# Kernel tuning notes

Hardware: AMD Instinct MI355X
Metric: run time of the kernel (lower is better)

## Reference

```python
import jax, jax.numpy as jnp
import numpy as np

EPS_OT = 0.1        # args.model.ot_reg
N_ITERS = 5         # args.model.ot_transport
COS_EPS = 1e-8      # torch F.cosine_similarity eps
L2_EPS = 1e-12      # torch F.normalize eps
LN_EPS = 1e-5       # nn.LayerNorm default eps
IN_DIM, HID = 768, 256


def setup_inputs() -> dict:
    key = jax.random.key(0)
    ks = jax.random.split(key, 8)
    Ba, Bb, Sa, Sb = 48, 48, 96, 96
    s_in = 1.0 / np.sqrt(IN_DIM)
    return {
        "batch_a": jax.random.normal(ks[0], (Ba, Sa, IN_DIM), jnp.float32),
        "batch_b": jax.random.normal(ks[1], (Bb, Sb, IN_DIM), jnp.float32),
        "Wq": jax.random.normal(ks[2], (IN_DIM, HID), jnp.float32) * s_in,
        "bq": jnp.zeros((HID,), jnp.float32),
        "Wk": jax.random.normal(ks[3], (IN_DIM, HID), jnp.float32) * s_in,
        "bk": jnp.zeros((HID,), jnp.float32),
        "Wv": jax.random.normal(ks[4], (IN_DIM, HID), jnp.float32) * s_in,
        "bv": jnp.zeros((HID,), jnp.float32),
        "ln_g": jnp.ones((HID,), jnp.float32),
        "ln_b": jnp.zeros((HID,), jnp.float32),
    }


def _layernorm(x, g, b):
    mu = jnp.mean(x, axis=-1, keepdims=True)
    var = jnp.var(x, axis=-1, keepdims=True)
    return (x - mu) * jax.lax.rsqrt(var + LN_EPS) * g + b


def _sinkhorn(C):
    # multiplicative Sinkhorn on kernel exp(C/eps); row/col renormalization
    T = jnp.exp(C / EPS_OT)  # [Ba,Bb,Sa,Sb]
    def body(_, T):
        T = T / jnp.sum(T, axis=-1, keepdims=True)
        T = T / jnp.sum(T, axis=-2, keepdims=True)
        return T
    return jax.lax.fori_loop(0, N_ITERS, body, T)


def reference(batch_a, batch_b, Wq, bq, Wk, bk, Wv, bv, ln_g, ln_b):
    q = batch_a @ Wq + bq          # [Ba,Sa,H]
    k = batch_b @ Wk + bk          # [Bb,Sb,H]
    v = batch_b @ Wv + bv          # [Bb,Sb,H]

    # cosine similarity across batches: [Ba,Bb,Sa,Sb]
    qn = q / jnp.maximum(jnp.linalg.norm(q, axis=-1, keepdims=True), COS_EPS)
    kn = k / jnp.maximum(jnp.linalg.norm(k, axis=-1, keepdims=True), COS_EPS)
    C = jnp.einsum('aid,bjd->abij', qn, kn)

    T = jax.lax.stop_gradient(_sinkhorn(C))  # C.detach() in source
    # F.normalize(dim=-1): L2 over last dim
    T = T / jnp.maximum(jnp.linalg.norm(T, axis=-1, keepdims=True), L2_EPS)
    # dropout p=0.0 -> identity (eval)

    attended = jnp.einsum('abij,bjd->abid', T, v) + q[:, None]  # [Ba,Bb,Sa,H]
    return _layernorm(attended, ln_g, ln_b)
```

## Files before the change

kernel.cpp:

```cpp
#include <hip/hip_runtime.h>
#include <hip/hip_bf16.h>

typedef __attribute__((ext_vector_type(4))) float f32x4;
typedef __attribute__((ext_vector_type(2))) float f32x2;
typedef __attribute__((ext_vector_type(8))) short bf16x8;
typedef __attribute__((ext_vector_type(4))) short s16x4;

#define BA 48
#define BB 48
#define SS 96
#define DIN 768
#define HH 256

static __device__ __forceinline__ short f2bf(float f) {
    __hip_bfloat16 h = __float2bfloat16(f);
    return *reinterpret_cast<short*>(&h);
}

static __device__ __forceinline__ f32x4 mfma16(bf16x8 a, bf16x8 b, f32x4 c) {
    return __builtin_amdgcn_mfma_f32_16x16x32_bf16(a, b, c, 0, 0, 0);
}

__global__ __launch_bounds__(256) void wt_kernel(
    const float* __restrict__ Wq, const float* __restrict__ Wk,
    const float* __restrict__ Wv, short* __restrict__ wt) {
    __shared__ float tile[64][65];
    int k0 = blockIdx.x * 64, n0 = blockIdx.y * 64, mat = blockIdx.z;
    const float* W = (mat == 0) ? Wq : (mat == 1) ? Wk : Wv;
    int t = threadIdx.x;
#pragma unroll
    for (int j = 0; j < 16; ++j) {
        int kk = j * 4 + (t >> 6);
        int nn = t & 63;
        tile[kk][nn] = W[(size_t)(k0 + kk) * HH + n0 + nn];
    }
    __syncthreads();
#pragma unroll
    for (int j = 0; j < 4; ++j) {
        int nn = j * 16 + (t >> 4);
        int kk = (t & 15) * 4;
        s16x4 pk;
#pragma unroll
        for (int i = 0; i < 4; ++i) pk[i] = f2bf(tile[kk + i][nn]);
        *reinterpret_cast<s16x4*>(&wt[(size_t)(mat * HH + n0 + nn) * DIN + k0 + kk]) = pk;
    }
}

__global__ __launch_bounds__(384) void qkv_kernel(
    const float* __restrict__ Xa, const float* __restrict__ Xb,
    const float* __restrict__ bq, const float* __restrict__ bk, const float* __restrict__ bv,
    const short* __restrict__ wt,
    float* __restrict__ q_ws, float* __restrict__ k_ws, short* __restrict__ vt_ws) {
    __shared__ short vtile[64][104];

    int bb = blockIdx.x;
    int mat = blockIdx.y;
    int c0 = blockIdx.z * 64;
    int tid = threadIdx.x;
    int wave = tid >> 6, lane = tid & 63;
    int c = lane & 15, g = lane >> 4;

    const float* X = ((mat == 0) ? Xa : Xb) + bb * SS * DIN;
    const short* Wt = wt + mat * HH * DIN;
    const float* bias = (mat == 0) ? bq : (mat == 1) ? bk : bv;

    const f32x4 z4 = {0.f, 0.f, 0.f, 0.f};
    f32x4 acc[4];
#pragma unroll
    for (int n = 0; n < 4; ++n) acc[n] = z4;

    const float* ap = X + (16 * wave + c) * DIN + g * 8;
    const short* bp = Wt + (c0 + c) * DIN + g * 8;
    for (int kk = 0; kk < DIN; kk += 32) {
        f32x4 a0 = *reinterpret_cast<const f32x4*>(ap + kk);
        f32x4 a1 = *reinterpret_cast<const f32x4*>(ap + kk + 4);
        bf16x8 af;
        af[0] = f2bf(a0[0]); af[1] = f2bf(a0[1]); af[2] = f2bf(a0[2]); af[3] = f2bf(a0[3]);
        af[4] = f2bf(a1[0]); af[5] = f2bf(a1[1]); af[6] = f2bf(a1[2]); af[7] = f2bf(a1[3]);
#pragma unroll
        for (int n = 0; n < 4; ++n) {
            bf16x8 bf = *reinterpret_cast<const bf16x8*>(bp + n * 16 * DIN + kk);
            acc[n] = mfma16(af, bf, acc[n]);
        }
    }
#pragma unroll
    for (int n = 0; n < 4; ++n) {
        float bv_ = bias[c0 + n * 16 + c];
#pragma unroll
        for (int r = 0; r < 4; ++r) acc[n][r] += bv_;
    }

    if (mat < 2) {
        float* dst = (mat == 0) ? q_ws : k_ws;
#pragma unroll
        for (int n = 0; n < 4; ++n)
#pragma unroll
            for (int r = 0; r < 4; ++r)
                dst[(bb * SS + 16 * wave + 4 * g + r) * HH + c0 + n * 16 + c] = acc[n][r];
    } else {
#pragma unroll
        for (int n = 0; n < 4; ++n)
#pragma unroll
            for (int r = 0; r < 4; ++r)
                vtile[n * 16 + c][16 * wave + 4 * g + r] = f2bf(acc[n][r]);
        __syncthreads();
#pragma unroll
        for (int t2 = 0; t2 < 2; ++t2) {
            int t = tid + t2 * 384;
            int d = t / 12, ch = t % 12;
            bf16x8 pk = *reinterpret_cast<const bf16x8*>(&vtile[d][ch * 8]);
            *reinterpret_cast<bf16x8*>(vt_ws + ((size_t)(bb * HH) + c0 + d) * SS + ch * 8) = pk;
        }
    }
}

__global__ __launch_bounds__(256) void norm_kernel(
    const float* __restrict__ q_ws, const float* __restrict__ k_ws,
    short* __restrict__ qn_ws, short* __restrict__ kn_ws) {
    int row = blockIdx.x * 4 + (threadIdx.x >> 6);
    int lane = threadIdx.x & 63;
    int isq = (row < 4608);
    const float* src = isq ? q_ws : k_ws;
    short* dst = isq ? qn_ws : kn_ws;
    int r = isq ? row : row - 4608;

    f32x4 v = *reinterpret_cast<const f32x4*>(src + (size_t)r * HH + lane * 4);
    float s = v[0] * v[0] + v[1] * v[1] + v[2] * v[2] + v[3] * v[3];
#pragma unroll
    for (int m = 1; m < 64; m <<= 1) s += __shfl_xor(s, m);
    float inv = 1.0f / fmaxf(sqrtf(s), 1e-8f);
    s16x4 o;
#pragma unroll
    for (int j = 0; j < 4; ++j) o[j] = f2bf(v[j] * inv);
    *reinterpret_cast<s16x4*>(dst + (size_t)r * HH + lane * 4) = o;
}

__global__ __launch_bounds__(256, 2) void sink_kernel(
    const short* __restrict__ qn_ws, const short* __restrict__ kn_ws,
    short* __restrict__ t_ws, int a_off) {
    int wave = threadIdx.x >> 6, lane = threadIdx.x & 63;
    int c = lane & 15, g = lane >> 4;
    int b = blockIdx.x * 4 + wave;
    int al = blockIdx.y;
    int a = al + a_off;

    const short* qbase = qn_ws + (size_t)(a * SS) * HH + c * HH + g * 8;
    const short* kbase = kn_ws + (size_t)(b * SS) * HH + c * HH + g * 8;

    const f32x4 z4 = {0.f, 0.f, 0.f, 0.f};
    f32x4 K[6][6];
#pragma unroll
    for (int ti = 0; ti < 6; ++ti)
#pragma unroll
        for (int tj = 0; tj < 6; ++tj) K[ti][tj] = z4;

#pragma unroll
    for (int kk = 0; kk < 8; ++kk) {
        bf16x8 qf[6];
#pragma unroll
        for (int ti = 0; ti < 6; ++ti)
            qf[ti] = *reinterpret_cast<const bf16x8*>(qbase + ti * 16 * HH + kk * 32);
#pragma unroll
        for (int tj = 0; tj < 6; ++tj) {
            bf16x8 kf = *reinterpret_cast<const bf16x8*>(kbase + tj * 16 * HH + kk * 32);
#pragma unroll
            for (int ti = 0; ti < 6; ++ti)
                K[ti][tj] = mfma16(kf, qf[ti], K[ti][tj]);
        }
    }

#pragma unroll
    for (int ti = 0; ti < 6; ++ti)
#pragma unroll
        for (int tj = 0; tj < 6; ++tj)
#pragma unroll
            for (int r = 0; r < 4; ++r)
                K[ti][tj][r] = exp2f(K[ti][tj][r] * 14.4269504088896341f);

#pragma unroll 1
    for (int it = 0; it < 5; ++it) {
#pragma unroll
        for (int ti = 0; ti < 6; ++ti) {
            float rs = 0.f;
#pragma unroll
            for (int tj = 0; tj < 6; ++tj)
                rs += K[ti][tj][0] + K[ti][tj][1] + K[ti][tj][2] + K[ti][tj][3];
            rs += __shfl_xor(rs, 16);
            rs += __shfl_xor(rs, 32);
            float rinv = 1.0f / rs;
#pragma unroll
            for (int tj = 0; tj < 6; ++tj)
#pragma unroll
                for (int r = 0; r < 4; ++r) K[ti][tj][r] *= rinv;
        }
        f32x4 cs[6];
#pragma unroll
        for (int tj = 0; tj < 6; ++tj) {
            cs[tj] = K[0][tj];
#pragma unroll
            for (int ti = 1; ti < 6; ++ti)
#pragma unroll
                for (int r = 0; r < 4; ++r) cs[tj][r] += K[ti][tj][r];
        }
#pragma unroll
        for (int m = 1; m < 16; m <<= 1)
#pragma unroll
            for (int tj = 0; tj < 6; ++tj)
#pragma unroll
                for (int r = 0; r < 4; ++r) cs[tj][r] += __shfl_xor(cs[tj][r], m);
#pragma unroll
        for (int tj = 0; tj < 6; ++tj) {
#pragma unroll
            for (int r = 0; r < 4; ++r) cs[tj][r] = 1.0f / cs[tj][r];
#pragma unroll
            for (int ti = 0; ti < 6; ++ti)
#pragma unroll
                for (int r = 0; r < 4; ++r) K[ti][tj][r] *= cs[tj][r];
        }
    }

    short* tp = t_ws + (size_t)(al * BB + b) * SS * SS;
#pragma unroll
    for (int ti = 0; ti < 6; ++ti) {
        float ss = 0.f;
#pragma unroll
        for (int tj = 0; tj < 6; ++tj)
#pragma unroll
            for (int r = 0; r < 4; ++r) ss += K[ti][tj][r] * K[ti][tj][r];
        ss += __shfl_xor(ss, 16);
        ss += __shfl_xor(ss, 32);
        float linv = 1.0f / fmaxf(sqrtf(ss), 1e-12f);
#pragma unroll
        for (int tj = 0; tj < 6; ++tj) {
            s16x4 pk;
#pragma unroll
            for (int r = 0; r < 4; ++r) pk[r] = f2bf(K[ti][tj][r] * linv);
            *reinterpret_cast<s16x4*>(tp + (16 * ti + c) * SS + 16 * tj + 4 * g) = pk;
        }
    }
}

__global__ __launch_bounds__(768, 6) void pv_kernel(
    const short* __restrict__ t_ws, const short* __restrict__ vt_ws,
    const float* __restrict__ q_ws,
    const float* __restrict__ ln_g, const float* __restrict__ ln_b,
    float* __restrict__ out, int a_off) {
    __shared__ float stats[2][2][SS];
    __shared__ float etile[12][4][136];

    int b = blockIdx.x, al = blockIdx.y;
    int a = al + a_off;
    int tid = threadIdx.x;
    int wave = tid >> 6, lane = tid & 63;
    int rt = wave % 6, h = wave / 6;
    int c = lane & 15, g = lane >> 4;

    const f32x4 z4 = {0.f, 0.f, 0.f, 0.f};
    f32x4 acc[8];
#pragma unroll
    for (int n = 0; n < 8; ++n) acc[n] = z4;

    const short* tp = t_ws + ((size_t)(al * BB + b)) * SS * SS + (16 * rt + c) * SS + g * 8;
    const short* vp = vt_ws + ((size_t)(b * HH) + 128 * h + c) * SS + g * 8;
#pragma unroll
    for (int ks = 0; ks < 3; ++ks) {
        bf16x8 af = *reinterpret_cast<const bf16x8*>(tp + ks * 32);
#pragma unroll
        for (int n = 0; n < 8; ++n) {
            bf16x8 bf = *reinterpret_cast<const bf16x8*>(vp + n * 16 * SS + ks * 32);
            acc[n] = mfma16(af, bf, acc[n]);
        }
    }

    const float* qa = q_ws + (size_t)a * SS * HH + 128 * h;
    int r0 = 16 * rt + 4 * g;
    float s1[4] = {0.f, 0.f, 0.f, 0.f};
    float s2[4] = {0.f, 0.f, 0.f, 0.f};
#pragma unroll
    for (int n = 0; n < 8; ++n)
#pragma unroll
        for (int r = 0; r < 4; ++r) {
            float x = acc[n][r] + qa[(r0 + r) * HH + n * 16 + c];
            acc[n][r] = x;
            s1[r] += x;
            s2[r] += x * x;
        }
#pragma unroll
    for (int m = 1; m < 16; m <<= 1)
#pragma unroll
        for (int r = 0; r < 4; ++r) {
            s1[r] += __shfl_xor(s1[r], m);
            s2[r] += __shfl_xor(s2[r], m);
        }
    if (c == 0) {
#pragma unroll
        for (int r = 0; r < 4; ++r) {
            stats[h][0][r0 + r] = s1[r];
            stats[h][1][r0 + r] = s2[r];
        }
    }
    __syncthreads();
    float mean[4], inv[4];
#pragma unroll
    for (int r = 0; r < 4; ++r) {
        float t1 = stats[0][0][r0 + r] + stats[1][0][r0 + r];
        float t2 = stats[0][1][r0 + r] + stats[1][1][r0 + r];
        mean[r] = t1 * (1.0f / 256.0f);
        float var = t2 * (1.0f / 256.0f) - mean[r] * mean[r];
        inv[r] = rsqrtf(var + 1e-5f);
    }

    f32x2 g2 = *reinterpret_cast<const f32x2*>(ln_g + 128 * h + 2 * lane);
    f32x2 b2 = *reinterpret_cast<const f32x2*>(ln_b + 128 * h + 2 * lane);
    float* ob = out + ((size_t)(a * BB + b)) * SS * HH + 128 * h;
#pragma unroll
    for (int r = 0; r < 4; ++r) {
#pragma unroll
        for (int n = 0; n < 8; ++n)
            etile[wave][g][n * 16 + c] = (acc[n][r] - mean[r]) * inv[r];
#pragma unroll
        for (int t = 0; t < 4; ++t) {
            f32x2 x2 = *reinterpret_cast<const f32x2*>(&etile[wave][t][2 * lane]);
            *reinterpret_cast<f32x2*>(ob + (size_t)(16 * rt + 4 * t + r) * HH + 2 * lane) =
                x2 * g2 + b2;
        }
    }
}

extern "C" void kernel_launch(void* const* d_in, const int* in_sizes, int n_in,
                              void* d_out, int out_size, void* d_ws, size_t ws_size,
                              hipStream_t stream) {
    const float* Xa = (const float*)d_in[0];
    const float* Xb = (const float*)d_in[1];
    const float* Wq = (const float*)d_in[2];
    const float* bq = (const float*)d_in[3];
    const float* Wk = (const float*)d_in[4];
    const float* bk = (const float*)d_in[5];
    const float* Wv = (const float*)d_in[6];
    const float* bv = (const float*)d_in[7];
    const float* ln_g = (const float*)d_in[8];
    const float* ln_b = (const float*)d_in[9];
    float* out = (float*)d_out;

    char* ws = (char*)d_ws;
    short* wt    = (short*)(ws);
    float* q_ws  = (float*)(ws + 1179648);
    float* k_ws  = (float*)(ws + 5898240);
    short* qn_ws = (short*)(ws + 10616832);
    short* kn_ws = (short*)(ws + 12976128);
    short* vt_ws = (short*)(ws + 15335424);

    const size_t t_full = (size_t)BA * BB * SS * SS * 2;
    size_t t_off = 17694720;
    size_t avail = (ws_size > t_off) ? ws_size - t_off : 0;
    int nch;
    if (avail >= t_full) nch = 1;
    else if (avail >= t_full / 2) nch = 2;
    else if (avail >= t_full / 4) nch = 4;
    else if (avail >= t_full / 8) nch = 8;
    else { nch = 16; t_off = 5898240; }
    short* t_ws = (short*)(ws + t_off);
    int apc = BA / nch;

    wt_kernel<<<dim3(12, 4, 3), dim3(256), 0, stream>>>(Wq, Wk, Wv, wt);
    qkv_kernel<<<dim3(BA, 3, 4), dim3(384), 0, stream>>>(Xa, Xb, bq, bk, bv, wt,
                                                         q_ws, k_ws, vt_ws);
    norm_kernel<<<dim3(2304), dim3(256), 0, stream>>>(q_ws, k_ws, qn_ws, kn_ws);
    for (int ch = 0; ch < nch; ++ch) {
        sink_kernel<<<dim3(12, apc), dim3(256), 0, stream>>>(qn_ws, kn_ws, t_ws, ch * apc);
        pv_kernel<<<dim3(BB, apc), dim3(768), 0, stream>>>(t_ws, vt_ws, q_ws,
                                                           ln_g, ln_b, out, ch * apc);
    }
}
```

Measured before the change: 252.5 us.

## Pre-cast inputs to bf16, raise sink occupancy, use nontemporal T loads and output stores

Adds a kernel that converts Xa and Xb to bf16 once, so the QKV GEMM loads bf16 fragments directly instead of re-converting fp32 in every block. The Sinkhorn kernel's occupancy hint goes from 2 to 3 blocks per CU, Q fragments are reloaded inside the inner loop to free registers, and the row, column and L2 reductions become tree-shaped. The PV kernel marks the transport-plan loads and the large fp32 output stores as nontemporal to reduce cache pollution. The workspace layout grows to hold the bf16 copies, and the small-workspace fallback now places T at offset 0, which would overwrite other buffers. The tighter register cap on the Sinkhorn kernel may cause spills.

```diff
diff --git a/kernel.cpp b/kernel.cpp
--- a/kernel.cpp
+++ b/kernel.cpp
@@ -46,8 +46,25 @@
     }
 }
 
+__global__ __launch_bounds__(256) void xbf_kernel(
+    const float* __restrict__ Xa, const float* __restrict__ Xb,
+    short* __restrict__ xa, short* __restrict__ xb) {
+    size_t i = (size_t)blockIdx.x * 256 + threadIdx.x;
+    const float* src;
+    short* dst;
+    size_t off;
+    if (i < 442368) { src = Xa; dst = xa; off = i * 8; }
+    else            { src = Xb; dst = xb; off = (i - 442368) * 8; }
+    f32x4 a = *reinterpret_cast<const f32x4*>(src + off);
+    f32x4 b = *reinterpret_cast<const f32x4*>(src + off + 4);
+    bf16x8 o;
+    o[0] = f2bf(a[0]); o[1] = f2bf(a[1]); o[2] = f2bf(a[2]); o[3] = f2bf(a[3]);
+    o[4] = f2bf(b[0]); o[5] = f2bf(b[1]); o[6] = f2bf(b[2]); o[7] = f2bf(b[3]);
+    *reinterpret_cast<bf16x8*>(dst + off) = o;
+}
+
 __global__ __launch_bounds__(384) void qkv_kernel(
-    const float* __restrict__ Xa, const float* __restrict__ Xb,
+    const short* __restrict__ xa, const short* __restrict__ xb,
     const float* __restrict__ bq, const float* __restrict__ bk, const float* __restrict__ bv,
     const short* __restrict__ wt,
     float* __restrict__ q_ws, float* __restrict__ k_ws, short* __restrict__ vt_ws) {
@@ -60,8 +77,8 @@
     int wave = tid >> 6, lane = tid & 63;
     int c = lane & 15, g = lane >> 4;
 
-    const float* X = ((mat == 0) ? Xa : Xb) + bb * SS * DIN;
-    const short* Wt = wt + mat * HH * DIN;
+    const short* X = ((mat == 0) ? xa : xb) + (size_t)bb * SS * DIN;
+    const short* Wt = wt + (size_t)mat * HH * DIN;
     const float* bias = (mat == 0) ? bq : (mat == 1) ? bk : bv;
 
     const f32x4 z4 = {0.f, 0.f, 0.f, 0.f};
@@ -69,14 +86,10 @@
 #pragma unroll
     for (int n = 0; n < 4; ++n) acc[n] = z4;
 
-    const float* ap = X + (16 * wave + c) * DIN + g * 8;
+    const short* ap = X + (16 * wave + c) * DIN + g * 8;
     const short* bp = Wt + (c0 + c) * DIN + g * 8;
     for (int kk = 0; kk < DIN; kk += 32) {
-        f32x4 a0 = *reinterpret_cast<const f32x4*>(ap + kk);
-        f32x4 a1 = *reinterpret_cast<const f32x4*>(ap + kk + 4);
-        bf16x8 af;
-        af[0] = f2bf(a0[0]); af[1] = f2bf(a0[1]); af[2] = f2bf(a0[2]); af[3] = f2bf(a0[3]);
-        af[4] = f2bf(a1[0]); af[5] = f2bf(a1[1]); af[6] = f2bf(a1[2]); af[7] = f2bf(a1[3]);
+        bf16x8 af = *reinterpret_cast<const bf16x8*>(ap + kk);
 #pragma unroll
         for (int n = 0; n < 4; ++n) {
             bf16x8 bf = *reinterpret_cast<const bf16x8*>(bp + n * 16 * DIN + kk);
@@ -135,7 +148,7 @@
     *reinterpret_cast<s16x4*>(dst + (size_t)r * HH + lane * 4) = o;
 }
 
-__global__ __launch_bounds__(256, 2) void sink_kernel(
+__global__ __launch_bounds__(256, 3) void sink_kernel(
     const short* __restrict__ qn_ws, const short* __restrict__ kn_ws,
     short* __restrict__ t_ws, int a_off) {
     int wave = threadIdx.x >> 6, lane = threadIdx.x & 63;
@@ -156,16 +169,14 @@
 
 #pragma unroll
     for (int kk = 0; kk < 8; ++kk) {
-        bf16x8 qf[6];
-#pragma unroll
-        for (int ti = 0; ti < 6; ++ti)
-            qf[ti] = *reinterpret_cast<const bf16x8*>(qbase + ti * 16 * HH + kk * 32);
 #pragma unroll
         for (int tj = 0; tj < 6; ++tj) {
             bf16x8 kf = *reinterpret_cast<const bf16x8*>(kbase + tj * 16 * HH + kk * 32);
 #pragma unroll
-            for (int ti = 0; ti < 6; ++ti)
-                K[ti][tj] = mfma16(kf, qf[ti], K[ti][tj]);
+            for (int ti = 0; ti < 6; ++ti) {
+                bf16x8 qf = *reinterpret_cast<const bf16x8*>(qbase + ti * 16 * HH + kk * 32);
+                K[ti][tj] = mfma16(kf, qf, K[ti][tj]);
+            }
         }
     }
 
@@ -181,10 +192,13 @@
     for (int it = 0; it < 5; ++it) {
 #pragma unroll
         for (int ti = 0; ti < 6; ++ti) {
-            float rs = 0.f;
-#pragma unroll
-            for (int tj = 0; tj < 6; ++tj)
-                rs += K[ti][tj][0] + K[ti][tj][1] + K[ti][tj][2] + K[ti][tj][3];
+            float s0 = (K[ti][0][0] + K[ti][0][1]) + (K[ti][0][2] + K[ti][0][3]);
+            float s1 = (K[ti][1][0] + K[ti][1][1]) + (K[ti][1][2] + K[ti][1][3]);
+            float s2 = (K[ti][2][0] + K[ti][2][1]) + (K[ti][2][2] + K[ti][2][3]);
+            float s3 = (K[ti][3][0] + K[ti][3][1]) + (K[ti][3][2] + K[ti][3][3]);
+            float s4 = (K[ti][4][0] + K[ti][4][1]) + (K[ti][4][2] + K[ti][4][3]);
+            float s5 = (K[ti][5][0] + K[ti][5][1]) + (K[ti][5][2] + K[ti][5][3]);
+            float rs = ((s0 + s1) + (s2 + s3)) + (s4 + s5);
             rs += __shfl_xor(rs, 16);
             rs += __shfl_xor(rs, 32);
             float rinv = 1.0f / rs;
@@ -193,40 +207,46 @@
 #pragma unroll
                 for (int r = 0; r < 4; ++r) K[ti][tj][r] *= rinv;
         }
-        f32x4 cs[6];
 #pragma unroll
         for (int tj = 0; tj < 6; ++tj) {
-            cs[tj] = K[0][tj];
-#pragma unroll
-            for (int ti = 1; ti < 6; ++ti)
-#pragma unroll
-                for (int r = 0; r < 4; ++r) cs[tj][r] += K[ti][tj][r];
-        }
-#pragma unroll
-        for (int m = 1; m < 16; m <<= 1)
-#pragma unroll
-            for (int tj = 0; tj < 6; ++tj)
-#pragma unroll
-                for (int r = 0; r < 4; ++r) cs[tj][r] += __shfl_xor(cs[tj][r], m);
-#pragma unroll
-        for (int tj = 0; tj < 6; ++tj) {
-#pragma unroll
-            for (int r = 0; r < 4; ++r) cs[tj][r] = 1.0f / cs[tj][r];
+            f32x4 cs;
+#pragma unroll
+            for (int r = 0; r < 4; ++r) {
+                float u0 = K[0][tj][r] + K[1][tj][r];
+                float u1 = K[2][tj][r] + K[3][tj][r];
+                float u2 = K[4][tj][r] + K[5][tj][r];
+                cs[r] = (u0 + u1) + u2;
+            }
+#pragma unroll
+            for (int m = 1; m < 16; m <<= 1)
+#pragma unroll
+                for (int r = 0; r < 4; ++r) cs[r] += __shfl_xor(cs[r], m);
+#pragma unroll
+            for (int r = 0; r < 4; ++r) cs[r] = 1.0f / cs[r];
 #pragma unroll
             for (int ti = 0; ti < 6; ++ti)
 #pragma unroll
-                for (int r = 0; r < 4; ++r) K[ti][tj][r] *= cs[tj][r];
+                for (int r = 0; r < 4; ++r) K[ti][tj][r] *= cs[r];
         }
     }
 
     short* tp = t_ws + (size_t)(al * BB + b) * SS * SS;
 #pragma unroll
     for (int ti = 0; ti < 6; ++ti) {
-        float ss = 0.f;
-#pragma unroll
-        for (int tj = 0; tj < 6; ++tj)
-#pragma unroll
-            for (int r = 0; r < 4; ++r) ss += K[ti][tj][r] * K[ti][tj][r];
+        float s0 = 0.f, s1 = 0.f, s2 = 0.f;
+#pragma unroll
+        for (int tj = 0; tj < 2; ++tj)
+#pragma unroll
+            for (int r = 0; r < 4; ++r) s0 += K[ti][tj][r] * K[ti][tj][r];
+#pragma unroll
+        for (int tj = 2; tj < 4; ++tj)
+#pragma unroll
+            for (int r = 0; r < 4; ++r) s1 += K[ti][tj][r] * K[ti][tj][r];
+#pragma unroll
+        for (int tj = 4; tj < 6; ++tj)
+#pragma unroll
+            for (int r = 0; r < 4; ++r) s2 += K[ti][tj][r] * K[ti][tj][r];
+        float ss = (s0 + s1) + s2;
         ss += __shfl_xor(ss, 16);
         ss += __shfl_xor(ss, 32);
         float linv = 1.0f / fmaxf(sqrtf(ss), 1e-12f);
@@ -264,7 +284,8 @@
     const short* vp = vt_ws + ((size_t)(b * HH) + 128 * h + c) * SS + g * 8;
 #pragma unroll
     for (int ks = 0; ks < 3; ++ks) {
-        bf16x8 af = *reinterpret_cast<const bf16x8*>(tp + ks * 32);
+        bf16x8 af = __builtin_nontemporal_load(
+            reinterpret_cast<const bf16x8*>(tp + ks * 32));
 #pragma unroll
         for (int n = 0; n < 8; ++n) {
             bf16x8 bf = *reinterpret_cast<const bf16x8*>(vp + n * 16 * SS + ks * 32);
@@ -321,8 +342,9 @@
 #pragma unroll
         for (int t = 0; t < 4; ++t) {
             f32x2 x2 = *reinterpret_cast<const f32x2*>(&etile[wave][t][2 * lane]);
-            *reinterpret_cast<f32x2*>(ob + (size_t)(16 * rt + 4 * t + r) * HH + 2 * lane) =
-                x2 * g2 + b2;
+            __builtin_nontemporal_store(
+                x2 * g2 + b2,
+                reinterpret_cast<f32x2*>(ob + (size_t)(16 * rt + 4 * t + r) * HH + 2 * lane));
         }
     }
 }
@@ -344,26 +366,28 @@
 
     char* ws = (char*)d_ws;
     short* wt    = (short*)(ws);
-    float* q_ws  = (float*)(ws + 1179648);
-    float* k_ws  = (float*)(ws + 5898240);
-    short* qn_ws = (short*)(ws + 10616832);
-    short* kn_ws = (short*)(ws + 12976128);
-    short* vt_ws = (short*)(ws + 15335424);
+    short* xa_bf = (short*)(ws + 1179648);
+    short* xb_bf = (short*)(ws + 8257536);
+    float* q_ws  = (float*)(ws + 15335424);
+    float* k_ws  = (float*)(ws + 20054016);
+    short* qn_ws = (short*)(ws + 24772608);
+    short* kn_ws = (short*)(ws + 27131904);
+    short* vt_ws = (short*)(ws + 29491200);
 
     const size_t t_full = (size_t)BA * BB * SS * SS * 2;
-    size_t t_off = 17694720;
+    size_t t_off = 31850496;
     size_t avail = (ws_size > t_off) ? ws_size - t_off : 0;
     int nch;
     if (avail >= t_full) nch = 1;
     else if (avail >= t_full / 2) nch = 2;
     else if (avail >= t_full / 4) nch = 4;
-    else if (avail >= t_full / 8) nch = 8;
-    else { nch = 16; t_off = 5898240; }
+    else { nch = 4; t_off = 0; }
     short* t_ws = (short*)(ws + t_off);
     int apc = BA / nch;
 
     wt_kernel<<<dim3(12, 4, 3), dim3(256), 0, stream>>>(Wq, Wk, Wv, wt);
-    qkv_kernel<<<dim3(BA, 3, 4), dim3(384), 0, stream>>>(Xa, Xb, bq, bk, bv, wt,
+    xbf_kernel<<<dim3(3456), dim3(256), 0, stream>>>(Xa, Xb, xa_bf, xb_bf);
+    qkv_kernel<<<dim3(BA, 3, 4), dim3(384), 0, stream>>>(xa_bf, xb_bf, bq, bk, bv, wt,
                                                          q_ws, k_ws, vt_ws);
     norm_kernel<<<dim3(2304), dim3(256), 0, stream>>>(q_ws, k_ws, qn_ws, kn_ws);
     for (int ch = 0; ch < nch; ++ch) {
```

Measured after the change: 395.7 us. 1.57x slower.
